# Kernel tuning notes

Measured on AMD Instinct MI355X. Metric: run time of the kernel, lower is better.

## Reference

```python
import jax, jax.numpy as jnp
import numpy as np

N = 50000        # nodes
F = 128          # input feature dim
U = 128          # units (output dim)
E_RAND = 1_600_000  # random edges; N self-loops appended -> E = 1_650_000
LABEL_IDXS = np.array([0, 5, 17, 42], dtype=np.int32)  # label_idxs init arg (indices into F)


def setup_inputs() -> dict:
    key = jax.random.key(0)
    k1, k2, k3, k4, k5 = jax.random.split(key, 5)
    x = jax.random.normal(k1, (1, N, F), dtype=jnp.float32)
    src = jax.random.randint(k2, (E_RAND,), 0, N, dtype=jnp.int32)
    dst = jax.random.randint(k3, (E_RAND,), 0, N, dtype=jnp.int32)
    # append self-loops so the diagonal of A (Adiag term) is nontrivial,
    # matching a normalized Laplacian which always has diagonal entries
    loops = jnp.arange(N, dtype=jnp.int32)
    edge_src = jnp.concatenate([src, loops])
    edge_dst = jnp.concatenate([dst, loops])
    edge_w = jax.random.uniform(k4, (E_RAND + N,), dtype=jnp.float32)
    kernel = jax.random.normal(k5, (F, U), dtype=jnp.float32) * (1.0 / np.sqrt(F))
    bias = jnp.zeros((U,), dtype=jnp.float32)
    return {"x": x, "edge_src": edge_src, "edge_dst": edge_dst,
            "edge_w": edge_w, "kernel": kernel, "bias": bias}


def reference(x, edge_src, edge_dst, edge_w, kernel, bias):
    # x: [1, N, F]; sparse A given as COO edges (edge_src=row i, edge_dst=col j, edge_w=A[i,j])
    n = x.shape[1]
    xs = x[0]  # [N, F]
    # A @ X  (sparse matmul via gather + segment_sum)
    agg = jax.ops.segment_sum(edge_w[:, None] * xs[edge_dst], edge_src, num_segments=n)  # [N, F]
    # diag(A): entries where row == col
    diag = jax.ops.segment_sum(jnp.where(edge_src == edge_dst, edge_w, jnp.float32(0.0)),
                               edge_src, num_segments=n)  # [N]
    # B = sum_{i in label_idxs} e_i e_i^T is a diagonal 0/1 selector on feature columns,
    # so (Adiag @ X) @ B == diag[:,None] * (X * mask)
    mask = jnp.zeros((xs.shape[1],), xs.dtype).at[jnp.asarray(LABEL_IDXS)].set(1.0)  # [F]
    h = agg - diag[:, None] * (xs * mask)  # [N, F]
    out = jax.nn.relu(h @ kernel + bias)   # [N, U]
    return out[None]  # [1, N, U]
```

## Files before the change

kernel.cpp:

```cpp
#include <hip/hip_runtime.h>

#define FDIM 128
#define UDIM 128
#define BROWS 32
#define CAP   1408
#define TILE  4096
#define EPT   16

typedef __attribute__((ext_vector_type(8))) short short8;
typedef __attribute__((ext_vector_type(4))) float floatx4;

__device__ inline unsigned int round_bf16_bits(float a) {
  unsigned int ua = __float_as_uint(a);
  ua += 0x7fffu + ((ua >> 16) & 1u);
  return ua & 0xffff0000u;
}
__device__ inline unsigned int pack_bf16(float a, float b) {
  unsigned int ua = __float_as_uint(a);
  unsigned int ub = __float_as_uint(b);
  ua += 0x7fffu + ((ua >> 16) & 1u);
  ub += 0x7fffu + ((ub >> 16) & 1u);
  return (ua >> 16) | (ub & 0xffff0000u);
}

__global__ __launch_bounds__(256) void prep(
    const float* __restrict__ K, uint4* __restrict__ kfrag,
    int* __restrict__ zbase, int zcount) {
  int gid = blockIdx.x * 256 + threadIdx.x;
  if (gid < 2048) {
    int lane = gid & 63, bb = gid >> 6;
    int n = (bb >> 2) * 16 + (lane & 15);
    int k0 = (bb & 3) * 32 + (lane >> 4) * 8;
    unsigned int pq[4];
    #pragma unroll
    for (int j = 0; j < 4; ++j) {
      float a = K[(size_t)(k0 + 2 * j) * UDIM + n];
      float b = K[(size_t)(k0 + 2 * j + 1) * UDIM + n];
      pq[j] = pack_bf16(a, b);
    }
    kfrag[gid] = make_uint4(pq[0], pq[1], pq[2], pq[3]);
  }
  if (gid < zcount) zbase[gid] = 0;
}

__device__ void bin_dev(int blk, const int* __restrict__ src,
                        const int* __restrict__ dst, const float* __restrict__ w,
                        int* __restrict__ cursor, uint2* __restrict__ meta,
                        float* __restrict__ diag, int E, int NB, char* smem) {
  int* scnt  = (int*)smem;
  int* sbase = scnt + NB;
  int* scur  = sbase + NB;
  int t = threadIdx.x;
  for (int b = t; b < NB; b += 256) { scnt[b] = 0; scur[b] = 0; }
  __syncthreads();

  uint2 pay[EPT];
  int e0 = blk * TILE;
  #pragma unroll
  for (int j = 0; j < EPT; ++j) {
    int e = e0 + j * 256 + t;
    if (e < E) {
      int s = src[e];
      int d = dst[e];
      float wv = w[e];
      if (s == d) atomicAdd(&diag[s], wv);
      pay[j].x = round_bf16_bits(wv) | (unsigned int)d;
      pay[j].y = (unsigned int)s;
      atomicAdd(&scnt[s >> 5], 1);
    } else {
      pay[j].y = 0xffffffffu;
    }
  }
  __syncthreads();

  for (int b = t; b < NB; b += 256) {
    int c = scnt[b];
    if (c) sbase[b] = b * CAP + atomicAdd(&cursor[b], c);
  }
  __syncthreads();

  #pragma unroll
  for (int j = 0; j < EPT; ++j) {
    if (pay[j].y != 0xffffffffu) {
      int b = (int)(pay[j].y >> 5);
      int r = atomicAdd(&scur[b], 1);
      int pos = sbase[b] + r;
      if (pos < (b + 1) * CAP)
        meta[pos] = make_uint2(pay[j].x, pay[j].y & 31u);
    }
  }
}

__device__ void gemm_dev(int g, const float* __restrict__ x,
                         const uint4* __restrict__ kfrag,
                         unsigned short* __restrict__ Ybf, int N, char* smem) {
  unsigned short (*sX)[136] = (unsigned short (*)[136])smem;
  int t = threadIdx.x;
  int r0 = g * 64;

  #pragma unroll
  for (int i = 0; i < 8; ++i) {
    int li = i * 256 + t;
    int row = li >> 5;
    int col4 = (li & 31) * 4;
    int gr = r0 + row; if (gr > N - 1) gr = N - 1;
    float4 v = *(const float4*)(x + (size_t)gr * FDIM + col4);
    *(uint2*)(&sX[row][col4]) = make_uint2(pack_bf16(v.x, v.y), pack_bf16(v.z, v.w));
  }
  __syncthreads();

  int wave = t >> 6, lane = t & 63;
  int m = lane & 15, q = lane >> 4;

  short8 bf[2][4];
  #pragma unroll
  for (int c = 0; c < 2; ++c)
    #pragma unroll
    for (int ks = 0; ks < 4; ++ks)
      bf[c][ks] = *(const short8*)&kfrag[(size_t)((2 * wave + c) * 4 + ks) * 64 + lane];

  floatx4 acc[4][2];
  #pragma unroll
  for (int rt = 0; rt < 4; ++rt)
    #pragma unroll
    for (int c = 0; c < 2; ++c)
      acc[rt][c] = (floatx4){0.f, 0.f, 0.f, 0.f};

  #pragma unroll
  for (int ks = 0; ks < 4; ++ks) {
    #pragma unroll
    for (int rt = 0; rt < 4; ++rt) {
      short8 af = *(const short8*)&sX[rt * 16 + m][ks * 32 + q * 8];
      acc[rt][0] = __builtin_amdgcn_mfma_f32_16x16x32_bf16(af, bf[0][ks], acc[rt][0], 0, 0, 0);
      acc[rt][1] = __builtin_amdgcn_mfma_f32_16x16x32_bf16(af, bf[1][ks], acc[rt][1], 0, 0, 0);
    }
  }

  #pragma unroll
  for (int rt = 0; rt < 4; ++rt) {
    #pragma unroll
    for (int c = 0; c < 2; ++c) {
      int col = (2 * wave + c) * 16 + m;
      #pragma unroll
      for (int reg = 0; reg < 4; ++reg) {
        int r = r0 + rt * 16 + q * 4 + reg;
        if (r < N)
          Ybf[(size_t)r * UDIM + col] =
              (unsigned short)(round_bf16_bits(acc[rt][c][reg]) >> 16);
      }
    }
  }
}

__global__ __launch_bounds__(256) void bin_gemm(
    const int* __restrict__ src, const int* __restrict__ dst,
    const float* __restrict__ w, int* __restrict__ cursor,
    uint2* __restrict__ meta, float* __restrict__ diag,
    const float* __restrict__ x, const uint4* __restrict__ kfrag,
    unsigned short* __restrict__ Ybf, int N, int E, int NB, int nbin) {
  __shared__ alignas(16) char smem[18816];
  if (blockIdx.x < (unsigned)nbin)
    bin_dev(blockIdx.x, src, dst, w, cursor, meta, diag, E, NB, smem);
  else
    gemm_dev(blockIdx.x - nbin, x, kfrag, Ybf, N, smem);
}

__global__ __launch_bounds__(256) void sort_gather(
    const unsigned short* __restrict__ Ybf, const uint2* __restrict__ meta,
    const int* __restrict__ cursor, const float* __restrict__ diag,
    const float* __restrict__ x, const float* __restrict__ K,
    const float* __restrict__ bias, float* __restrict__ out, int N) {
  __shared__ unsigned int sdstw[CAP];
  __shared__ unsigned int sorted[CAP];
  __shared__ unsigned char skey[CAP];
  __shared__ int kcnt[BROWS];
  __shared__ int rstart[BROWS + 1];
  int b = blockIdx.x;
  int t = threadIdx.x;
  int cntE = cursor[b]; if (cntE > CAP) cntE = CAP;
  const uint2* mb = meta + (size_t)b * CAP;

  if (t < BROWS) kcnt[t] = 0;
  __syncthreads();

  for (int e = t; e < cntE; e += 256) {
    uint2 m = mb[e];
    sdstw[e] = m.x;
    skey[e] = (unsigned char)m.y;
    atomicAdd(&kcnt[m.y & 31u], 1);
  }
  __syncthreads();

  if (t < BROWS) {
    int v = kcnt[t];
    int incl = v;
    #pragma unroll
    for (int off = 1; off < BROWS; off <<= 1) {
      int u = __shfl_up(incl, off, 64);
      if (t >= off) incl += u;
    }
    rstart[t + 1] = incl;
    kcnt[t] = incl - v;
    if (t == 0) rstart[0] = 0;
  }
  __syncthreads();

  for (int e = t; e < cntE; e += 256) {
    int k = skey[e];
    int pos = atomicAdd(&kcnt[k], 1);
    sorted[pos] = sdstw[e];
  }
  __syncthreads();

  int lane = t & 63, sub = lane & 31;
  int slot = (t >> 6) * 2 + (lane >> 5);
  for (int p = 0; p < 4; ++p) {
    int rl = p * 8 + slot;
    int g = b * BROWS + rl;
    int base = rstart[rl], end = rstart[rl + 1];

    float4 acc = {0.f, 0.f, 0.f, 0.f};
    int i = base;
    for (; i + 8 <= end; i += 8) {
      unsigned int mi[8];
      #pragma unroll
      for (int j = 0; j < 8; ++j) mi[j] = sorted[i + j];
      uint2 pk[8];
      #pragma unroll
      for (int j = 0; j < 8; ++j)
        pk[j] = *(const uint2*)(Ybf + (size_t)(mi[j] & 0xffffu) * UDIM + sub * 4);
      #pragma unroll
      for (int j = 0; j < 8; ++j) {
        float wj = __uint_as_float(mi[j] & 0xffff0000u);
        acc.x += wj * __uint_as_float(pk[j].x << 16);
        acc.y += wj * __uint_as_float(pk[j].x & 0xffff0000u);
        acc.z += wj * __uint_as_float(pk[j].y << 16);
        acc.w += wj * __uint_as_float(pk[j].y & 0xffff0000u);
      }
    }
    for (; i < end; ++i) {
      unsigned int mi = sorted[i];
      float wj = __uint_as_float(mi & 0xffff0000u);
      uint2 pk = *(const uint2*)(Ybf + (size_t)(mi & 0xffffu) * UDIM + sub * 4);
      acc.x += wj * __uint_as_float(pk.x << 16);
      acc.y += wj * __uint_as_float(pk.x & 0xffff0000u);
      acc.z += wj * __uint_as_float(pk.y << 16);
      acc.w += wj * __uint_as_float(pk.y & 0xffff0000u);
    }

    if (g < N) {
      float dg = diag[g];
      const int lf[4] = {0, 5, 17, 42};
      #pragma unroll
      for (int tt = 0; tt < 4; ++tt) {
        float c = dg * x[(size_t)g * FDIM + lf[tt]];
        float4 k4 = *(const float4*)(K + (size_t)lf[tt] * UDIM + sub * 4);
        acc.x -= c * k4.x; acc.y -= c * k4.y;
        acc.z -= c * k4.z; acc.w -= c * k4.w;
      }
      float4 b4 = *(const float4*)(bias + sub * 4);
      acc.x = fmaxf(acc.x + b4.x, 0.f);
      acc.y = fmaxf(acc.y + b4.y, 0.f);
      acc.z = fmaxf(acc.z + b4.z, 0.f);
      acc.w = fmaxf(acc.w + b4.w, 0.f);
      *(float4*)(out + (size_t)g * UDIM + sub * 4) = acc;
    }
  }
}

extern "C" void kernel_launch(void* const* d_in, const int* in_sizes, int n_in,
                              void* d_out, int out_size, void* d_ws, size_t ws_size,
                              hipStream_t stream) {
  const float* x    = (const float*)d_in[0];
  const int*   esrc = (const int*)d_in[1];
  const int*   edst = (const int*)d_in[2];
  const float* ew   = (const float*)d_in[3];
  const float* K    = (const float*)d_in[4];
  const float* bias = (const float*)d_in[5];
  float* out = (float*)d_out;

  const int N = in_sizes[0] / FDIM;
  const int E = in_sizes[1];
  const int NB = (N + BROWS - 1) / BROWS;

  char* p = (char*)d_ws;
  unsigned short* Ybf = (unsigned short*)p; p += (size_t)N * UDIM * 2;
  float* diag  = (float*)p;         p += (size_t)N * 4;
  int*   cursor = (int*)p;          p += (size_t)NB * 4;
  uint4* kfrag = (uint4*)p;         p += (size_t)32 * 64 * 16;
  uint2* meta = (uint2*)p;          p += (size_t)NB * CAP * 8;

  const int nbin = (E + TILE - 1) / TILE;
  const int ngemm = (N + 63) / 64;

  prep<<<(N + NB + 255) / 256, 256, 0, stream>>>(K, kfrag, (int*)diag, N + NB);
  bin_gemm<<<nbin + ngemm, 256, 0, stream>>>(
      esrc, edst, ew, cursor, meta, diag, x, kfrag, Ybf, N, E, NB, nbin);
  sort_gather<<<NB, 256, 0, stream>>>(Ybf, meta, cursor, diag, x, K, bias, out, N);
}
```

Before: 179.4 us.

## Fuse prep, binning, GEMM and gather into one persistent kernel with flags

Merges the three kernel launches into a single launch whose blocks take roles (kfrag prep, edge binning, GEMM, sort/gather) and coordinate through global atomic flag counters with spin-waits, replacing the zeroing kernel with a memset. The binning tile is also doubled (TILE 8192, EPT 32) to halve the number of binning blocks. This aims to remove launch gaps and let the gather phase overlap with the tail of the earlier phases. In exchange it depends on blocks being dispatched in index order, since a gather block that spins before the producer blocks are resident could deadlock, and the spin-waiting occupies compute slots.

```diff
diff --git a/kernel.cpp b/kernel.cpp
--- a/kernel.cpp
+++ b/kernel.cpp
@@ -4,8 +4,9 @@
 #define UDIM 128
 #define BROWS 32
 #define CAP   1408
-#define TILE  4096
-#define EPT   16
+#define TILE  8192
+#define EPT   32
+#define NPREP 8
 
 typedef __attribute__((ext_vector_type(8))) short short8;
 typedef __attribute__((ext_vector_type(4))) float floatx4;
@@ -23,24 +24,13 @@
   return (ua >> 16) | (ub & 0xffff0000u);
 }
 
-__global__ __launch_bounds__(256) void prep(
-    const float* __restrict__ K, uint4* __restrict__ kfrag,
-    int* __restrict__ zbase, int zcount) {
-  int gid = blockIdx.x * 256 + threadIdx.x;
-  if (gid < 2048) {
-    int lane = gid & 63, bb = gid >> 6;
-    int n = (bb >> 2) * 16 + (lane & 15);
-    int k0 = (bb & 3) * 32 + (lane >> 4) * 8;
-    unsigned int pq[4];
-    #pragma unroll
-    for (int j = 0; j < 4; ++j) {
-      float a = K[(size_t)(k0 + 2 * j) * UDIM + n];
-      float b = K[(size_t)(k0 + 2 * j + 1) * UDIM + n];
-      pq[j] = pack_bf16(a, b);
-    }
-    kfrag[gid] = make_uint4(pq[0], pq[1], pq[2], pq[3]);
-  }
-  if (gid < zcount) zbase[gid] = 0;
+__device__ inline void wait_flag(int* f, int target) {
+  while (atomicAdd(f, 0) < target) __builtin_amdgcn_s_sleep(32);
+  __threadfence();
+}
+__device__ inline void signal_flag(int* f) {
+  __threadfence();
+  atomicAdd(f, 1);
 }
 
 __device__ void bin_dev(int blk, const int* __restrict__ src,
@@ -152,36 +142,26 @@
   }
 }
 
-__global__ __launch_bounds__(256) void bin_gemm(
-    const int* __restrict__ src, const int* __restrict__ dst,
-    const float* __restrict__ w, int* __restrict__ cursor,
-    uint2* __restrict__ meta, float* __restrict__ diag,
-    const float* __restrict__ x, const uint4* __restrict__ kfrag,
-    unsigned short* __restrict__ Ybf, int N, int E, int NB, int nbin) {
-  __shared__ alignas(16) char smem[18816];
-  if (blockIdx.x < (unsigned)nbin)
-    bin_dev(blockIdx.x, src, dst, w, cursor, meta, diag, E, NB, smem);
-  else
-    gemm_dev(blockIdx.x - nbin, x, kfrag, Ybf, N, smem);
-}
-
-__global__ __launch_bounds__(256) void sort_gather(
-    const unsigned short* __restrict__ Ybf, const uint2* __restrict__ meta,
-    const int* __restrict__ cursor, const float* __restrict__ diag,
-    const float* __restrict__ x, const float* __restrict__ K,
-    const float* __restrict__ bias, float* __restrict__ out, int N) {
-  __shared__ unsigned int sdstw[CAP];
-  __shared__ unsigned int sorted[CAP];
-  __shared__ unsigned char skey[CAP];
-  __shared__ int kcnt[BROWS];
-  __shared__ int rstart[BROWS + 1];
-  int b = blockIdx.x;
+__device__ void sort_gather_dev(
+    int b, const unsigned short* __restrict__ Ybf,
+    const uint2* __restrict__ meta, const int* __restrict__ cursor,
+    const float* __restrict__ diag, const float* __restrict__ x,
+    const float* __restrict__ K, const float* __restrict__ bias,
+    float* __restrict__ out, int N, int* flags, int nbin, int ngemm,
+    char* smem) {
+  unsigned int* sdstw = (unsigned int*)smem;
+  unsigned int* sorted = (unsigned int*)(smem + 5632);
+  unsigned char* skey = (unsigned char*)(smem + 11264);
+  int* kcnt = (int*)(smem + 12672);
+  int* rstart = (int*)(smem + 12800);
   int t = threadIdx.x;
+
+  if (t == 0) wait_flag(&flags[1], nbin);
+  if (t < BROWS) kcnt[t] = 0;
+  __syncthreads();
+
   int cntE = cursor[b]; if (cntE > CAP) cntE = CAP;
   const uint2* mb = meta + (size_t)b * CAP;
-
-  if (t < BROWS) kcnt[t] = 0;
-  __syncthreads();
 
   for (int e = t; e < cntE; e += 256) {
     uint2 m = mb[e];
@@ -210,6 +190,8 @@
     int pos = atomicAdd(&kcnt[k], 1);
     sorted[pos] = sdstw[e];
   }
+
+  if (t == 0) wait_flag(&flags[2], ngemm);
   __syncthreads();
 
   int lane = t & 63, sub = lane & 31;
@@ -268,6 +250,50 @@
   }
 }
 
+__global__ __launch_bounds__(256) void fused_all(
+    const int* __restrict__ src, const int* __restrict__ dst,
+    const float* __restrict__ w, const float* __restrict__ x,
+    const float* __restrict__ K, const float* __restrict__ bias,
+    float* __restrict__ out, float* __restrict__ diag,
+    int* __restrict__ cursor, int* __restrict__ flags,
+    uint4* __restrict__ kfrag, uint2* __restrict__ meta,
+    unsigned short* __restrict__ Ybf,
+    int N, int E, int NB, int nbin, int ngemm) {
+  __shared__ alignas(16) char smem[18816];
+  int b = blockIdx.x;
+  int t = threadIdx.x;
+
+  if (b < NPREP) {
+    int gid = b * 256 + t;
+    int lane = gid & 63, bb = gid >> 6;
+    int n = (bb >> 2) * 16 + (lane & 15);
+    int k0 = (bb & 3) * 32 + (lane >> 4) * 8;
+    unsigned int pq[4];
+    #pragma unroll
+    for (int j = 0; j < 4; ++j) {
+      float a = K[(size_t)(k0 + 2 * j) * UDIM + n];
+      float bfv = K[(size_t)(k0 + 2 * j + 1) * UDIM + n];
+      pq[j] = pack_bf16(a, bfv);
+    }
+    kfrag[gid] = make_uint4(pq[0], pq[1], pq[2], pq[3]);
+    __syncthreads();
+    if (t == 0) signal_flag(&flags[0]);
+  } else if (b < NPREP + nbin) {
+    bin_dev(b - NPREP, src, dst, w, cursor, meta, diag, E, NB, smem);
+    __syncthreads();
+    if (t == 0) signal_flag(&flags[1]);
+  } else if (b < NPREP + nbin + ngemm) {
+    if (t == 0) wait_flag(&flags[0], NPREP);
+    __syncthreads();
+    gemm_dev(b - NPREP - nbin, x, kfrag, Ybf, N, smem);
+    __syncthreads();
+    if (t == 0) signal_flag(&flags[2]);
+  } else {
+    sort_gather_dev(b - NPREP - nbin - ngemm, Ybf, meta, cursor, diag, x, K,
+                    bias, out, N, flags, nbin, ngemm, smem);
+  }
+}
+
 extern "C" void kernel_launch(void* const* d_in, const int* in_sizes, int n_in,
                               void* d_out, int out_size, void* d_ws, size_t ws_size,
                               hipStream_t stream) {
@@ -287,14 +313,15 @@
   unsigned short* Ybf = (unsigned short*)p; p += (size_t)N * UDIM * 2;
   float* diag  = (float*)p;         p += (size_t)N * 4;
   int*   cursor = (int*)p;          p += (size_t)NB * 4;
+  int*   flags = (int*)p;           p += 4 * 4;
   uint4* kfrag = (uint4*)p;         p += (size_t)32 * 64 * 16;
   uint2* meta = (uint2*)p;          p += (size_t)NB * CAP * 8;
 
   const int nbin = (E + TILE - 1) / TILE;
   const int ngemm = (N + 63) / 64;
 
-  prep<<<(N + NB + 255) / 256, 256, 0, stream>>>(K, kfrag, (int*)diag, N + NB);
-  bin_gemm<<<nbin + ngemm, 256, 0, stream>>>(
-      esrc, edst, ew, cursor, meta, diag, x, kfrag, Ybf, N, E, NB, nbin);
-  sort_gather<<<NB, 256, 0, stream>>>(Ybf, meta, cursor, diag, x, K, bias, out, N);
-}
+  hipMemsetAsync(diag, 0, ((size_t)N + NB + 4) * 4, stream);
+  fused_all<<<NPREP + nbin + ngemm + NB, 256, 0, stream>>>(
+      esrc, edst, ew, x, K, bias, out, diag, cursor, flags, kfrag, meta, Ybf,
+      N, E, NB, nbin, ngemm);
+}
```

Measured after the change: 395.5 us. +120.5%, slower.

## Drop prep kernel: pack weights inside GEMM blocks, memset workspace, unroll gather by 16

Applied to the files above, without the earlier changes.

Removes the separate prep kernel. Each GEMM block now loads and packs the kernel weights to bf16 fragments itself, placed before the barrier so the loads overlap the X tile staging, and the diag/cursor zeroing becomes a hipMemsetAsync. It also adds a 16-wide unrolled gather loop in sort_gather so more Ybf loads are in flight per row. This removes one kernel launch and an extra workspace round-trip, at the cost of redundant strided K reads in every GEMM block and higher register pressure in the gather.

```diff
diff --git a/kernel.cpp b/kernel.cpp
--- a/kernel.cpp
+++ b/kernel.cpp
@@ -21,26 +21,6 @@
   ua += 0x7fffu + ((ua >> 16) & 1u);
   ub += 0x7fffu + ((ub >> 16) & 1u);
   return (ua >> 16) | (ub & 0xffff0000u);
-}
-
-__global__ __launch_bounds__(256) void prep(
-    const float* __restrict__ K, uint4* __restrict__ kfrag,
-    int* __restrict__ zbase, int zcount) {
-  int gid = blockIdx.x * 256 + threadIdx.x;
-  if (gid < 2048) {
-    int lane = gid & 63, bb = gid >> 6;
-    int n = (bb >> 2) * 16 + (lane & 15);
-    int k0 = (bb & 3) * 32 + (lane >> 4) * 8;
-    unsigned int pq[4];
-    #pragma unroll
-    for (int j = 0; j < 4; ++j) {
-      float a = K[(size_t)(k0 + 2 * j) * UDIM + n];
-      float b = K[(size_t)(k0 + 2 * j + 1) * UDIM + n];
-      pq[j] = pack_bf16(a, b);
-    }
-    kfrag[gid] = make_uint4(pq[0], pq[1], pq[2], pq[3]);
-  }
-  if (gid < zcount) zbase[gid] = 0;
 }
 
 __device__ void bin_dev(int blk, const int* __restrict__ src,
@@ -92,7 +72,7 @@
 }
 
 __device__ void gemm_dev(int g, const float* __restrict__ x,
-                         const uint4* __restrict__ kfrag,
+                         const float* __restrict__ K,
                          unsigned short* __restrict__ Ybf, int N, char* smem) {
   unsigned short (*sX)[136] = (unsigned short (*)[136])smem;
   int t = threadIdx.x;
@@ -107,17 +87,26 @@
     float4 v = *(const float4*)(x + (size_t)gr * FDIM + col4);
     *(uint2*)(&sX[row][col4]) = make_uint2(pack_bf16(v.x, v.y), pack_bf16(v.z, v.w));
   }
-  __syncthreads();
 
   int wave = t >> 6, lane = t & 63;
   int m = lane & 15, q = lane >> 4;
 
   short8 bf[2][4];
   #pragma unroll
-  for (int c = 0; c < 2; ++c)
-    #pragma unroll
-    for (int ks = 0; ks < 4; ++ks)
-      bf[c][ks] = *(const short8*)&kfrag[(size_t)((2 * wave + c) * 4 + ks) * 64 + lane];
+  for (int c = 0; c < 2; ++c) {
+    int n = (2 * wave + c) * 16 + m;
+    #pragma unroll
+    for (int ks = 0; ks < 4; ++ks) {
+      int k0 = ks * 32 + q * 8;
+      uint4 pq;
+      pq.x = pack_bf16(K[(size_t)(k0 + 0) * UDIM + n], K[(size_t)(k0 + 1) * UDIM + n]);
+      pq.y = pack_bf16(K[(size_t)(k0 + 2) * UDIM + n], K[(size_t)(k0 + 3) * UDIM + n]);
+      pq.z = pack_bf16(K[(size_t)(k0 + 4) * UDIM + n], K[(size_t)(k0 + 5) * UDIM + n]);
+      pq.w = pack_bf16(K[(size_t)(k0 + 6) * UDIM + n], K[(size_t)(k0 + 7) * UDIM + n]);
+      bf[c][ks] = *(short8*)&pq;
+    }
+  }
+  __syncthreads();
 
   floatx4 acc[4][2];
   #pragma unroll
@@ -156,13 +145,13 @@
     const int* __restrict__ src, const int* __restrict__ dst,
     const float* __restrict__ w, int* __restrict__ cursor,
     uint2* __restrict__ meta, float* __restrict__ diag,
-    const float* __restrict__ x, const uint4* __restrict__ kfrag,
+    const float* __restrict__ x, const float* __restrict__ K,
     unsigned short* __restrict__ Ybf, int N, int E, int NB, int nbin) {
   __shared__ alignas(16) char smem[18816];
   if (blockIdx.x < (unsigned)nbin)
     bin_dev(blockIdx.x, src, dst, w, cursor, meta, diag, E, NB, smem);
   else
-    gemm_dev(blockIdx.x - nbin, x, kfrag, Ybf, N, smem);
+    gemm_dev(blockIdx.x - nbin, x, K, Ybf, N, smem);
 }
 
 __global__ __launch_bounds__(256) void sort_gather(
@@ -221,6 +210,23 @@
 
     float4 acc = {0.f, 0.f, 0.f, 0.f};
     int i = base;
+    for (; i + 16 <= end; i += 16) {
+      unsigned int mi[16];
+      #pragma unroll
+      for (int j = 0; j < 16; ++j) mi[j] = sorted[i + j];
+      uint2 pk[16];
+      #pragma unroll
+      for (int j = 0; j < 16; ++j)
+        pk[j] = *(const uint2*)(Ybf + (size_t)(mi[j] & 0xffffu) * UDIM + sub * 4);
+      #pragma unroll
+      for (int j = 0; j < 16; ++j) {
+        float wj = __uint_as_float(mi[j] & 0xffff0000u);
+        acc.x += wj * __uint_as_float(pk[j].x << 16);
+        acc.y += wj * __uint_as_float(pk[j].x & 0xffff0000u);
+        acc.z += wj * __uint_as_float(pk[j].y << 16);
+        acc.w += wj * __uint_as_float(pk[j].y & 0xffff0000u);
+      }
+    }
     for (; i + 8 <= end; i += 8) {
       unsigned int mi[8];
       #pragma unroll
@@ -287,14 +293,13 @@
   unsigned short* Ybf = (unsigned short*)p; p += (size_t)N * UDIM * 2;
   float* diag  = (float*)p;         p += (size_t)N * 4;
   int*   cursor = (int*)p;          p += (size_t)NB * 4;
-  uint4* kfrag = (uint4*)p;         p += (size_t)32 * 64 * 16;
   uint2* meta = (uint2*)p;          p += (size_t)NB * CAP * 8;
 
   const int nbin = (E + TILE - 1) / TILE;
   const int ngemm = (N + 63) / 64;
 
-  prep<<<(N + NB + 255) / 256, 256, 0, stream>>>(K, kfrag, (int*)diag, N + NB);
+  hipMemsetAsync(diag, 0, ((size_t)N + NB) * 4, stream);
   bin_gemm<<<nbin + ngemm, 256, 0, stream>>>(
-      esrc, edst, ew, cursor, meta, diag, x, kfrag, Ybf, N, E, NB, nbin);
+      esrc, edst, ew, cursor, meta, diag, x, K, Ybf, N, E, NB, nbin);
   sort_gather<<<NB, 256, 0, stream>>>(Ybf, meta, cursor, diag, x, K, bias, out, N);
 }
```

Result: slower. 190.1 us (+6.0%).
